# Optimization experiments

Hardware: AMD Instinct MI355X
Metric: run time of the kernel (lower is better)

## Reference

```python
import jax, jax.numpy as jnp
import numpy as np

NEG_SLOPE = 0.2
EPS = 1e-16


def setup_inputs() -> dict:
    key = jax.random.key(0)
    k = jax.random.split(key, 6)
    N, K, D_IN, D_OUT = 20000, 32, 256, 256
    nodes = jax.random.normal(k[0], (N, D_IN), dtype=jnp.float32)
    neighbors = jax.random.normal(k[1], (N, K, D_IN), dtype=jnp.float32)
    # xavier-uniform-ish scales for faithfulness to init_params
    lim_w = float(np.sqrt(6.0 / (D_IN + D_OUT)))
    W = jax.random.uniform(k[2], (D_OUT, D_IN), minval=-lim_w, maxval=lim_w, dtype=jnp.float32)
    lim_a = float(np.sqrt(6.0 / (1 + D_OUT)))
    a_src = jax.random.uniform(k[3], (D_OUT,), minval=-lim_a, maxval=lim_a, dtype=jnp.float32)
    a_tgt = jax.random.uniform(k[4], (D_OUT,), minval=-lim_a, maxval=lim_a, dtype=jnp.float32)
    bias = jnp.zeros((D_OUT,), dtype=jnp.float32)
    return {"nodes": nodes, "neighbors": neighbors, "W": W, "a_src": a_src, "a_tgt": a_tgt, "bias": bias}


def reference(nodes, neighbors, W, a_src, a_tgt, bias):
    # GAT layer (num_of_heads=1), eval mode (dropout = identity).
    # nodes: [N, D_in], neighbors: [N, K, D_in]
    nodes_proj = nodes @ W.T                              # [N, D_out]
    scores_t = nodes_proj @ a_tgt                         # [N]
    neigh_proj = jnp.einsum('nkf,of->nko', neighbors, W)  # [N, K, D_out]
    scores_s = neigh_proj @ a_src                         # [N, K]
    e = scores_s + scores_t[:, None]                      # per-edge raw score
    e = jnp.where(e >= 0, e, NEG_SLOPE * e)               # leakyReLU(0.2)
    exp_e = jnp.exp(e)                                    # original uses raw exp (no max-subtract)
    attn = exp_e / (jnp.sum(exp_e, axis=1, keepdims=True) + EPS)  # [N, K]
    out = jnp.einsum('nk,nko->no', attn, neigh_proj)      # weighted sum over neighbors
    out = out + bias
    return jax.nn.elu(out)                                # activation = ELU
```

## Files before the change

kernel.cpp:

```cpp
#include <hip/hip_runtime.h>
#include <hip/hip_bf16.h>
#include <math.h>

#define D 256
#define KNB 32
#define NEG_SLOPE 0.2f

#define PART_OFF 53280
#define AGG_OFF  69664

using bfrag = __attribute__((ext_vector_type(8))) short;
using ffrag = __attribute__((ext_vector_type(4))) float;

__device__ __forceinline__ unsigned short f2bf(float x) {
    __hip_bfloat16 h = __float2bfloat16(x);
    return *reinterpret_cast<unsigned short*>(&h);
}

__global__ __launch_bounds__(256) void prep1_kernel(
    const float* __restrict__ W, const float* __restrict__ a_src,
    const float* __restrict__ a_tgt, float* __restrict__ ws)
{
    int t = threadIdx.x;
    int b = blockIdx.x;
    if (b < 64) {
        float4 v = reinterpret_cast<const float4*>(W)[b * 256 + t];
        ushort4 u;
        u.x = f2bf(v.x); u.y = f2bf(v.y); u.z = f2bf(v.z); u.w = f2bf(v.w);
        reinterpret_cast<ushort4*>(ws + 512)[b * 256 + t] = u;
    } else {
        int bb = b - 64;
        float ps = 0.f, pt = 0.f;
        #pragma unroll
        for (int oo = 0; oo < 8; ++oo) {
            int o = bb * 8 + oo;
            float wv = W[o * D + t];
            ps = fmaf(a_src[o], wv, ps);
            pt = fmaf(a_tgt[o], wv, pt);
        }
        ws[PART_OFF + bb * 256 + t]        = ps;
        ws[PART_OFF + 8192 + bb * 256 + t] = pt;
    }
}

__global__ __launch_bounds__(256) void prep2_kernel(float* __restrict__ ws)
{
    int t = threadIdx.x;
    float s = 0.f, g = 0.f;
    #pragma unroll
    for (int j = 0; j < 32; ++j) {
        s += ws[PART_OFF + j * 256 + t];
        g += ws[PART_OFF + 8192 + j * 256 + t];
    }
    ws[t]     = s;
    ws[D + t] = g;
}

__global__ __launch_bounds__(256) void scores_t_kernel(
    const float* __restrict__ nodes, const float* __restrict__ ws,
    float* __restrict__ scores_t, int N)
{
    int wid  = threadIdx.x >> 6;
    int lane = threadIdx.x & 63;
    int n = blockIdx.x * 4 + wid;
    if (n >= N) return;
    float4 v = reinterpret_cast<const float4*>(nodes + (size_t)n * D)[lane];
    float4 w = reinterpret_cast<const float4*>(ws + D)[lane];
    float s = v.x * w.x + v.y * w.y + v.z * w.z + v.w * w.w;
    #pragma unroll
    for (int off = 1; off < 64; off <<= 1) s += __shfl_xor(s, off);
    if (lane == 0) scores_t[n] = s;
}

__global__ __launch_bounds__(256) void attn_agg_kernel(
    const float* __restrict__ neighbors, const float* __restrict__ ws,
    const float* __restrict__ scores_t, unsigned short* __restrict__ aggbf, int N)
{
    __shared__ __align__(16) float4 part[16][64];
    __shared__ __align__(16) float4 part2[4][64];
    __shared__ float wsum[4];

    const int t   = threadIdx.x;
    const int n   = blockIdx.x;
    const int w   = t >> 6;
    const int s   = (t >> 4) & 3;
    const int c16 = t & 15;
    const int g   = t >> 4;
    const int R   = 8 * w + 2 * s;

    const float4* tile = reinterpret_cast<const float4*>(
        neighbors + (size_t)n * (KNB * D));
    float4 v[8];
    #pragma unroll
    for (int j = 0; j < 8; ++j)
        v[j] = tile[(R + (j >> 2)) * 64 + (j & 3) * 16 + c16];

    const float4* ws4 = reinterpret_cast<const float4*>(ws);
    float4 wsv[4];
    #pragma unroll
    for (int m = 0; m < 4; ++m) wsv[m] = ws4[m * 16 + c16];

    const float st = scores_t[n];

    float pA = 0.f, pB = 0.f;
    #pragma unroll
    for (int m = 0; m < 4; ++m) {
        pA = fmaf(v[m].x, wsv[m].x, fmaf(v[m].y, wsv[m].y,
             fmaf(v[m].z, wsv[m].z, fmaf(v[m].w, wsv[m].w, pA))));
        pB = fmaf(v[4+m].x, wsv[m].x, fmaf(v[4+m].y, wsv[m].y,
             fmaf(v[4+m].z, wsv[m].z, fmaf(v[4+m].w, wsv[m].w, pB))));
    }
    #pragma unroll
    for (int off = 1; off < 16; off <<= 1) {
        pA += __shfl_xor(pA, off);
        pB += __shfl_xor(pB, off);
    }

    float eA = pA + st; eA = (eA >= 0.f) ? eA : NEG_SLOPE * eA;
    float eB = pB + st; eB = (eB >= 0.f) ? eB : NEG_SLOPE * eB;
    float xA = __expf(eA);
    float xB = __expf(eB);

    float gs = xA + xB;
    gs += __shfl_xor(gs, 16);
    gs += __shfl_xor(gs, 32);
    if ((t & 63) == 0) wsum[w] = gs;

    #pragma unroll
    for (int m = 0; m < 4; ++m) {
        float4 a;
        a.x = fmaf(xA, v[m].x, xB * v[4+m].x);
        a.y = fmaf(xA, v[m].y, xB * v[4+m].y);
        a.z = fmaf(xA, v[m].z, xB * v[4+m].z);
        a.w = fmaf(xA, v[m].w, xB * v[4+m].w);
        part[g][(m * 16 + c16) ^ ((g & 3) << 1)] = a;
    }
    __syncthreads();

    {
        int q = t & 63, gg = t >> 6;
        float4 sum = part[gg * 4 + 0][q ^ 0];
        float4 b1  = part[gg * 4 + 1][q ^ 2];
        float4 b2  = part[gg * 4 + 2][q ^ 4];
        float4 b3  = part[gg * 4 + 3][q ^ 6];
        sum.x += b1.x + b2.x + b3.x;
        sum.y += b1.y + b2.y + b3.y;
        sum.z += b1.z + b2.z + b3.z;
        sum.w += b1.w + b2.w + b3.w;
        part2[gg][q] = sum;
    }
    __syncthreads();

    if (t < 64) {
        float4 a0 = part2[0][t], a1 = part2[1][t], a2 = part2[2][t], a3 = part2[3][t];
        float inv = 1.f / (wsum[0] + wsum[1] + wsum[2] + wsum[3] + 1e-16f);
        float4 r;
        r.x = (a0.x + a1.x + a2.x + a3.x) * inv;
        r.y = (a0.y + a1.y + a2.y + a3.y) * inv;
        r.z = (a0.z + a1.z + a2.z + a3.z) * inv;
        r.w = (a0.w + a1.w + a2.w + a3.w) * inv;
        ushort4 u;
        u.x = f2bf(r.x); u.y = f2bf(r.y); u.z = f2bf(r.z); u.w = f2bf(r.w);
        reinterpret_cast<ushort4*>(aggbf + (size_t)n * D)[t] = u;
    }
}

__global__ __launch_bounds__(64) void out_gemm_kernel(
    const unsigned short* __restrict__ aggbf,
    const unsigned short* __restrict__ wbf,
    const float* __restrict__ bias, float* __restrict__ out, int N)
{
    int l = threadIdx.x;
    int m0 = blockIdx.x * 16;
    if (m0 >= N) return;
    int lr = l & 15, lk = l >> 4;

    ffrag acc[16];
    #pragma unroll
    for (int nf = 0; nf < 16; ++nf) acc[nf] = ffrag{0.f, 0.f, 0.f, 0.f};

    #pragma unroll
    for (int ks = 0; ks < 8; ++ks) {
        bfrag a = *reinterpret_cast<const bfrag*>(
            aggbf + (size_t)(m0 + lr) * D + ks * 32 + lk * 8);
        #pragma unroll
        for (int nf = 0; nf < 16; ++nf) {
            bfrag b = *reinterpret_cast<const bfrag*>(
                wbf + (size_t)(nf * 16 + lr) * D + ks * 32 + lk * 8);
            acc[nf] = __builtin_amdgcn_mfma_f32_16x16x32_bf16(a, b, acc[nf], 0, 0, 0);
        }
    }

    #pragma unroll
    for (int nf = 0; nf < 16; ++nf) {
        int col = nf * 16 + lr;
        float bv = bias[col];
        #pragma unroll
        for (int r = 0; r < 4; ++r) {
            int m = m0 + lk * 4 + r;
            float x = acc[nf][r] + bv;
            x = (x > 0.f) ? x : expm1f(x);
            out[(size_t)m * D + col] = x;
        }
    }
}

extern "C" void kernel_launch(void* const* d_in, const int* in_sizes, int n_in,
                              void* d_out, int out_size, void* d_ws, size_t ws_size,
                              hipStream_t stream) {
    const float* nodes     = (const float*)d_in[0];
    const float* neighbors = (const float*)d_in[1];
    const float* W         = (const float*)d_in[2];
    const float* a_src     = (const float*)d_in[3];
    const float* a_tgt     = (const float*)d_in[4];
    const float* bias      = (const float*)d_in[5];
    float* out = (float*)d_out;
    float* ws  = (float*)d_ws;

    int N = in_sizes[0] / D;
    unsigned short* wbf   = (unsigned short*)(ws + 512);
    float* scores_t       = ws + 33280;
    unsigned short* aggbf = (unsigned short*)(ws + AGG_OFF);

    hipLaunchKernelGGL(prep1_kernel, dim3(96), dim3(256), 0, stream,
                       W, a_src, a_tgt, ws);
    hipLaunchKernelGGL(prep2_kernel, dim3(1), dim3(256), 0, stream, ws);
    hipLaunchKernelGGL(scores_t_kernel, dim3((N + 3) / 4), dim3(256), 0, stream,
                       nodes, ws, scores_t, N);
    hipLaunchKernelGGL(attn_agg_kernel, dim3(N), dim3(256), 0, stream,
                       neighbors, ws, scores_t, aggbf, N);
    hipLaunchKernelGGL(out_gemm_kernel, dim3(N / 16), dim3(64), 0, stream,
                       aggbf, wbf, bias, out, N);
}
```

Before: 185.9 us.

## Process two nodes per block in attention aggregation with transposed reduction

```diff
diff --git a/kernel.cpp b/kernel.cpp
--- a/kernel.cpp
+++ b/kernel.cpp
@@ -72,96 +72,137 @@
     if (lane == 0) scores_t[n] = s;
 }
 
+__device__ __forceinline__ float xreduce8(const float* p, int lane)
+{
+    bool b0 = lane & 1, b1 = lane & 2, b2 = lane & 4;
+    float s0_0 = (b0 ? p[1] : p[0]) + __shfl_xor(b0 ? p[0] : p[1], 1);
+    float s0_1 = (b0 ? p[3] : p[2]) + __shfl_xor(b0 ? p[2] : p[3], 1);
+    float s0_2 = (b0 ? p[5] : p[4]) + __shfl_xor(b0 ? p[4] : p[5], 1);
+    float s0_3 = (b0 ? p[7] : p[6]) + __shfl_xor(b0 ? p[6] : p[7], 1);
+    float s1_0 = (b1 ? s0_1 : s0_0) + __shfl_xor(b1 ? s0_0 : s0_1, 2);
+    float s1_1 = (b1 ? s0_3 : s0_2) + __shfl_xor(b1 ? s0_2 : s0_3, 2);
+    float s2   = (b2 ? s1_1 : s1_0) + __shfl_xor(b2 ? s1_0 : s1_1, 4);
+    s2 += __shfl_xor(s2, 8);
+    s2 += __shfl_xor(s2, 16);
+    s2 += __shfl_xor(s2, 32);
+    return s2;
+}
+
 __global__ __launch_bounds__(256) void attn_agg_kernel(
     const float* __restrict__ neighbors, const float* __restrict__ ws,
     const float* __restrict__ scores_t, unsigned short* __restrict__ aggbf, int N)
 {
-    __shared__ __align__(16) float4 part[16][64];
-    __shared__ __align__(16) float4 part2[4][64];
-    __shared__ float wsum[4];
-
-    const int t   = threadIdx.x;
-    const int n   = blockIdx.x;
-    const int w   = t >> 6;
-    const int s   = (t >> 4) & 3;
-    const int c16 = t & 15;
-    const int g   = t >> 4;
-    const int R   = 8 * w + 2 * s;
-
-    const float4* tile = reinterpret_cast<const float4*>(
-        neighbors + (size_t)n * (KNB * D));
-    float4 v[8];
-    #pragma unroll
-    for (int j = 0; j < 8; ++j)
-        v[j] = tile[(R + (j >> 2)) * 64 + (j & 3) * 16 + c16];
-
-    const float4* ws4 = reinterpret_cast<const float4*>(ws);
-    float4 wsv[4];
-    #pragma unroll
-    for (int m = 0; m < 4; ++m) wsv[m] = ws4[m * 16 + c16];
-
-    const float st = scores_t[n];
-
-    float pA = 0.f, pB = 0.f;
-    #pragma unroll
-    for (int m = 0; m < 4; ++m) {
-        pA = fmaf(v[m].x, wsv[m].x, fmaf(v[m].y, wsv[m].y,
-             fmaf(v[m].z, wsv[m].z, fmaf(v[m].w, wsv[m].w, pA))));
-        pB = fmaf(v[4+m].x, wsv[m].x, fmaf(v[4+m].y, wsv[m].y,
-             fmaf(v[4+m].z, wsv[m].z, fmaf(v[4+m].w, wsv[m].w, pB))));
-    }
-    #pragma unroll
-    for (int off = 1; off < 16; off <<= 1) {
-        pA += __shfl_xor(pA, off);
-        pB += __shfl_xor(pB, off);
-    }
-
-    float eA = pA + st; eA = (eA >= 0.f) ? eA : NEG_SLOPE * eA;
-    float eB = pB + st; eB = (eB >= 0.f) ? eB : NEG_SLOPE * eB;
-    float xA = __expf(eA);
-    float xB = __expf(eB);
-
-    float gs = xA + xB;
-    gs += __shfl_xor(gs, 16);
-    gs += __shfl_xor(gs, 32);
-    if ((t & 63) == 0) wsum[w] = gs;
-
-    #pragma unroll
-    for (int m = 0; m < 4; ++m) {
-        float4 a;
-        a.x = fmaf(xA, v[m].x, xB * v[4+m].x);
-        a.y = fmaf(xA, v[m].y, xB * v[4+m].y);
-        a.z = fmaf(xA, v[m].z, xB * v[4+m].z);
-        a.w = fmaf(xA, v[m].w, xB * v[4+m].w);
-        part[g][(m * 16 + c16) ^ ((g & 3) << 1)] = a;
+    __shared__ float spA[KNB], spB[KNB];
+    __shared__ float wsumA[4], wsumB[4];
+    __shared__ __align__(16) float4 part2A[4][64];
+    __shared__ __align__(16) float4 part2B[4][64];
+
+    const int t    = threadIdx.x;
+    const int lane = t & 63;
+    const int w    = t >> 6;
+    const int nA   = blockIdx.x * 2;
+    const bool hasB = (nA + 1 < N);
+    const int nB   = hasB ? nA + 1 : nA;
+
+    const float4 wsv = reinterpret_cast<const float4*>(ws)[lane];
+    const float stA = scores_t[nA];
+    const float stB = scores_t[nB];
+
+    const float4* tA = reinterpret_cast<const float4*>(neighbors + (size_t)nA * (KNB * D));
+    const float4* tB = reinterpret_cast<const float4*>(neighbors + (size_t)nB * (KNB * D));
+
+    float4 vA[8], vB[8];
+    #pragma unroll
+    for (int i = 0; i < 8; ++i) vA[i] = tA[(8 * w + i) * 64 + lane];
+    #pragma unroll
+    for (int i = 0; i < 8; ++i) vB[i] = tB[(8 * w + i) * 64 + lane];
+
+    {
+        float p[8];
+        #pragma unroll
+        for (int i = 0; i < 8; ++i)
+            p[i] = fmaf(vA[i].x, wsv.x, fmaf(vA[i].y, wsv.y,
+                   fmaf(vA[i].z, wsv.z, vA[i].w * wsv.w)));
+        float s2 = xreduce8(p, lane);
+        float e = s2 + stA; e = (e >= 0.f) ? e : NEG_SLOPE * e;
+        float x = __expf(e);
+        float d = x + __shfl_xor(x, 1);
+        d += __shfl_xor(d, 2);
+        d += __shfl_xor(d, 4);
+        if (lane < 8) spA[8 * w + lane] = x;
+        if (lane == 0) wsumA[w] = d;
+    }
+    {
+        float p[8];
+        #pragma unroll
+        for (int i = 0; i < 8; ++i)
+            p[i] = fmaf(vB[i].x, wsv.x, fmaf(vB[i].y, wsv.y,
+                   fmaf(vB[i].z, wsv.z, vB[i].w * wsv.w)));
+        float s2 = xreduce8(p, lane);
+        float e = s2 + stB; e = (e >= 0.f) ? e : NEG_SLOPE * e;
+        float x = __expf(e);
+        float d = x + __shfl_xor(x, 1);
+        d += __shfl_xor(d, 2);
+        d += __shfl_xor(d, 4);
+        if (lane < 8) spB[8 * w + lane] = x;
+        if (lane == 0) wsumB[w] = d;
     }
     __syncthreads();
 
     {
-        int q = t & 63, gg = t >> 6;
-        float4 sum = part[gg * 4 + 0][q ^ 0];
-        float4 b1  = part[gg * 4 + 1][q ^ 2];
-        float4 b2  = part[gg * 4 + 2][q ^ 4];
-        float4 b3  = part[gg * 4 + 3][q ^ 6];
-        sum.x += b1.x + b2.x + b3.x;
-        sum.y += b1.y + b2.y + b3.y;
-        sum.z += b1.z + b2.z + b3.z;
-        sum.w += b1.w + b2.w + b3.w;
-        part2[gg][q] = sum;
+        float xw[8];
+        #pragma unroll
+        for (int i = 0; i < 8; ++i) xw[i] = spA[8 * w + i];
+        float4 acc = make_float4(0.f, 0.f, 0.f, 0.f);
+        #pragma unroll
+        for (int i = 0; i < 8; ++i) {
+            acc.x = fmaf(xw[i], vA[i].x, acc.x);
+            acc.y = fmaf(xw[i], vA[i].y, acc.y);
+            acc.z = fmaf(xw[i], vA[i].z, acc.z);
+            acc.w = fmaf(xw[i], vA[i].w, acc.w);
+        }
+        part2A[w][lane] = acc;
+    }
+    {
+        float xw[8];
+        #pragma unroll
+        for (int i = 0; i < 8; ++i) xw[i] = spB[8 * w + i];
+        float4 acc = make_float4(0.f, 0.f, 0.f, 0.f);
+        #pragma unroll
+        for (int i = 0; i < 8; ++i) {
+            acc.x = fmaf(xw[i], vB[i].x, acc.x);
+            acc.y = fmaf(xw[i], vB[i].y, acc.y);
+            acc.z = fmaf(xw[i], vB[i].z, acc.z);
+            acc.w = fmaf(xw[i], vB[i].w, acc.w);
+        }
+        part2B[w][lane] = acc;
     }
     __syncthreads();
 
-    if (t < 64) {
-        float4 a0 = part2[0][t], a1 = part2[1][t], a2 = part2[2][t], a3 = part2[3][t];
-        float inv = 1.f / (wsum[0] + wsum[1] + wsum[2] + wsum[3] + 1e-16f);
+    if (w == 0) {
+        float4 q0 = part2A[0][lane], q1 = part2A[1][lane];
+        float4 q2 = part2A[2][lane], q3 = part2A[3][lane];
+        float inv = 1.f / (wsumA[0] + wsumA[1] + wsumA[2] + wsumA[3] + 1e-16f);
         float4 r;
-        r.x = (a0.x + a1.x + a2.x + a3.x) * inv;
-        r.y = (a0.y + a1.y + a2.y + a3.y) * inv;
-        r.z = (a0.z + a1.z + a2.z + a3.z) * inv;
-        r.w = (a0.w + a1.w + a2.w + a3.w) * inv;
+        r.x = (q0.x + q1.x + q2.x + q3.x) * inv;
+        r.y = (q0.y + q1.y + q2.y + q3.y) * inv;
+        r.z = (q0.z + q1.z + q2.z + q3.z) * inv;
+        r.w = (q0.w + q1.w + q2.w + q3.w) * inv;
         ushort4 u;
         u.x = f2bf(r.x); u.y = f2bf(r.y); u.z = f2bf(r.z); u.w = f2bf(r.w);
-        reinterpret_cast<ushort4*>(aggbf + (size_t)n * D)[t] = u;
+        reinterpret_cast<ushort4*>(aggbf + (size_t)nA * D)[lane] = u;
+    } else if (w == 1 && hasB) {
+        float4 q0 = part2B[0][lane], q1 = part2B[1][lane];
+        float4 q2 = part2B[2][lane], q3 = part2B[3][lane];
+        float inv = 1.f / (wsumB[0] + wsumB[1] + wsumB[2] + wsumB[3] + 1e-16f);
+        float4 r;
+        r.x = (q0.x + q1.x + q2.x + q3.x) * inv;
+        r.y = (q0.y + q1.y + q2.y + q3.y) * inv;
+        r.z = (q0.z + q1.z + q2.z + q3.z) * inv;
+        r.w = (q0.w + q1.w + q2.w + q3.w) * inv;
+        ushort4 u;
+        u.x = f2bf(r.x); u.y = f2bf(r.y); u.z = f2bf(r.z); u.w = f2bf(r.w);
+        reinterpret_cast<ushort4*>(aggbf + (size_t)nB * D)[lane] = u;
     }
 }
 
@@ -227,8 +268,8 @@
     hipLaunchKernelGGL(prep2_kernel, dim3(1), dim3(256), 0, stream, ws);
     hipLaunchKernelGGL(scores_t_kernel, dim3((N + 3) / 4), dim3(256), 0, stream,
                        nodes, ws, scores_t, N);
-    hipLaunchKernelGGL(attn_agg_kernel, dim3(N), dim3(256), 0, stream,
+    hipLaunchKernelGGL(attn_agg_kernel, dim3((N + 1) / 2), dim3(256), 0, stream,
                        neighbors, ws, scores_t, aggbf, N);
-    hipLaunchKernelGGL(out_gemm_kernel, dim3(N / 16), dim3(64), 0, stream,
+    hipLaunchKernelGGL(out_gemm_kernel, dim3((N + 15) / 16), dim3(64), 0, stream,
                        aggbf, wbf, bias, out, N);
 }
```

Result: slower. 191.1 us (+2.8%).
